# Optimization experiments

Measured on AMD Instinct MI355X. Metric: run time of the kernel, lower is better.

The kernel has to match this reference:

```python
import jax, jax.numpy as jnp
import numpy as np

B, N, M = 16, 4096, 1024
C2, C1 = 256, 128          # points2 channels (in_channel), points1 channels
MLP = [256, 256]
IN0 = C2 + C1              # use_points1=True concat


def setup_inputs() -> dict:
    key = jax.random.key(0)
    ks = jax.random.split(key, 8)
    inp = {
        "xyz1": jax.random.normal(ks[0], (B, 3, N), jnp.float32),
        "xyz2": jax.random.normal(ks[1], (B, 3, M), jnp.float32),
        "points1": jax.random.normal(ks[2], (B, C1, N), jnp.float32),
        "points2": jax.random.normal(ks[3], (B, C2, M), jnp.float32),
        # 1x1 Conv1d weights == dense matrices (out, in)
        "W1": jax.random.normal(ks[4], (MLP[0], IN0), jnp.float32) / np.sqrt(IN0),
        "b1": jnp.zeros((MLP[0],), jnp.float32),
        "W2": jax.random.normal(ks[5], (MLP[1], MLP[0]), jnp.float32) / np.sqrt(MLP[0]),
        "b2": jnp.zeros((MLP[1],), jnp.float32),
    }
    return inp


def _fp(xyz1, xyz2, points1, points2, W1, b1, W2, b2):
    # three_nn: squared pairwise distances via ||a||^2 + ||b||^2 - 2 a.b
    # xyz*: (B, 3, N/M)
    sq1 = jnp.sum(xyz1 * xyz1, axis=1)                 # (B, N)
    sq2 = jnp.sum(xyz2 * xyz2, axis=1)                 # (B, M)
    inner = jnp.einsum("bcn,bcm->bnm", xyz1, xyz2)     # (B, N, M)
    d2 = sq1[:, :, None] + sq2[:, None, :] - 2.0 * inner
    neg_d2, idx = jax.lax.top_k(-d2, 3)                # 3 smallest -> (B, N, 3)
    dist = jnp.sqrt(jnp.maximum(-neg_d2, 1e-20))       # Euclidean, like three_nn wrapper
    dist = jnp.maximum(dist, 1e-10)                    # torch.clamp_min
    recip = 1.0 / dist
    weight = recip / jnp.sum(recip, axis=2, keepdims=True)  # (B, N, 3)
    # three_interpolate: gather points2 at idx and weighted-sum
    gathered = jax.vmap(lambda p, i: p[:, i])(points2, idx)  # (B, C2, N, 3)
    interp = jnp.einsum("bcnk,bnk->bcn", gathered, weight)   # (B, C2, N)
    x = jnp.concatenate([interp, points1], axis=1)           # (B, C2+C1, N)
    # mlp_conv: 1x1 conv + relu (if_bn=False)
    x = jax.nn.relu(jnp.einsum("oc,bcn->bon", W1, x) + b1[None, :, None])
    x = jax.nn.relu(jnp.einsum("oc,bcn->bon", W2, x) + b2[None, :, None])
    return x


def reference(xyz1, xyz2, points1, points2, W1, b1, W2, b2):
    return _fp(xyz1, xyz2, points1, points2, W1, b1, W2, b2)
```

## Files before the change

kernel.cpp:

```cpp
#include <hip/hip_runtime.h>

#define B_  16
#define N_  4096
#define M_  1024
#define C1_ 128
#define C2_ 256
#define K0_ 384
#define O1_ 256
#define O2_ 256

typedef _Float16 half4  __attribute__((ext_vector_type(4)));
typedef _Float16 half8  __attribute__((ext_vector_type(8)));
typedef float    f32x4  __attribute__((ext_vector_type(4)));

__global__ __launch_bounds__(256)
void three_nn_kernel(const float* __restrict__ xyz1, const float* __restrict__ xyz2,
                     int* __restrict__ idxb, float* __restrict__ wb) {
    __shared__ float pts[8 * 516];
    int b = blockIdx.y;
    int t = threadIdx.x;
    {
        const float* src = xyz2 + (size_t)b * 3 * M_;
        int m0 = t * 4;
        f32x4 xv = *(const f32x4*)(src + m0);
        f32x4 yv = *(const f32x4*)(src + M_ + m0);
        f32x4 zv = *(const f32x4*)(src + 2 * M_ + m0);
        float* dst = pts + (m0 >> 7) * 516 + (m0 & 127) * 4;
#pragma unroll
        for (int jj = 0; jj < 4; ++jj) {
            f32x4 o = {xv[jj], yv[jj], zv[jj],
                       fmaf(xv[jj], xv[jj], fmaf(yv[jj], yv[jj], zv[jj] * zv[jj]))};
            *(f32x4*)(dst + jj * 4) = o;
        }
    }
    __syncthreads();
    int lane = t & 63;
    int c = lane & 7;
    int q = ((t >> 6) << 3) + (lane >> 3);
    int n = blockIdx.x * 32 + q;
    const float* qp = xyz1 + (size_t)b * 3 * N_;
    float px = qp[n], py = qp[N_ + n], pz = qp[2 * N_ + n];
    float px2 = -2.f * px, py2 = -2.f * py, pz2 = -2.f * pz;
    const float* base = pts + c * 516;
    float b0 = 1e30f, b1v = 1e30f, b2v = 1e30f;
    int i0 = 0, i1 = 0, i2 = 0;
    int mb = c * 128;
#pragma unroll 4
    for (int i = 0; i < 128; ++i) {
        f32x4 pv = *(const f32x4*)(base + i * 4);
        float d = fmaf(pv[0], px2, fmaf(pv[1], py2, fmaf(pv[2], pz2, pv[3])));
        int m = mb + i;
        bool c0 = d < b0, c1 = d < b1v, c2 = d < b2v;
        float nb1 = __builtin_amdgcn_fmed3f(d, b0, b1v);
        float nb2 = __builtin_amdgcn_fmed3f(d, b1v, b2v);
        i2 = c1 ? i1 : (c2 ? m : i2);
        i1 = c0 ? i0 : (c1 ? m : i1);
        i0 = c0 ? m : i0;
        b0 = fminf(b0, d);
        b1v = nb1; b2v = nb2;
    }
#pragma unroll
    for (int st = 1; st <= 4; st <<= 1) {
        float d0 = __shfl_xor(b0, st, 64);  int j0 = __shfl_xor(i0, st, 64);
        float d1 = __shfl_xor(b1v, st, 64); int j1 = __shfl_xor(i1, st, 64);
        float d2 = __shfl_xor(b2v, st, 64); int j2 = __shfl_xor(i2, st, 64);
#pragma unroll
        for (int e = 0; e < 3; ++e) {
            float d = (e == 0) ? d0 : (e == 1) ? d1 : d2;
            int   m = (e == 0) ? j0 : (e == 1) ? j1 : j2;
            bool c0 = d < b0, c1 = d < b1v, c2 = d < b2v;
            float nb1 = __builtin_amdgcn_fmed3f(d, b0, b1v);
            float nb2 = __builtin_amdgcn_fmed3f(d, b1v, b2v);
            i2 = c1 ? i1 : (c2 ? m : i2);
            i1 = c0 ? i0 : (c1 ? m : i1);
            i0 = c0 ? m : i0;
            b0 = fminf(b0, d);
            b1v = nb1; b2v = nb2;
        }
    }
    if ((lane & 7) == 0) {
        float sq1 = fmaf(px, px, fmaf(py, py, pz * pz));
        float e0 = fmaxf(sqrtf(fmaxf(b0 + sq1, 1e-20f)), 1e-10f);
        float e1 = fmaxf(sqrtf(fmaxf(b1v + sq1, 1e-20f)), 1e-10f);
        float e2 = fmaxf(sqrtf(fmaxf(b2v + sq1, 1e-20f)), 1e-10f);
        float r0 = 1.f / e0, r1 = 1.f / e1, r2 = 1.f / e2;
        float s = r0 + r1 + r2;
        size_t j = ((size_t)b * N_ + n) * 3;
        idxb[j] = i0; idxb[j + 1] = i1; idxb[j + 2] = i2;
        wb[j] = r0 / s; wb[j + 1] = r1 / s; wb[j + 2] = r2 / s;
    }
}

__global__ __launch_bounds__(256)
void convert_w_kernel(const float* __restrict__ W1, const float* __restrict__ W2,
                      _Float16* __restrict__ W1h, _Float16* __restrict__ W2h) {
    int t = blockIdx.x * 256 + threadIdx.x;
    if (t < O1_ * K0_) W1h[t] = (_Float16)W1[t];
    if (t < O2_ * O1_) W2h[t] = (_Float16)W2[t];
}

__global__ __launch_bounds__(256)
void transpose_f16_kernel(const float* __restrict__ in, _Float16* __restrict__ out,
                          int NP, size_t in_bstride, size_t out_bstride,
                          int out_rstride) {
    __shared__ float tile[64][65];
    int t = threadIdx.x;
    int nb = blockIdx.x * 64, cb = blockIdx.y * 64;
    const float* ib = in + blockIdx.z * in_bstride;
#pragma unroll
    for (int r = 0; r < 16; ++r) {
        int cc = r * 4 + (t >> 6);
        tile[cc][t & 63] = ib[(size_t)(cb + cc) * NP + nb + (t & 63)];
    }
    __syncthreads();
    _Float16* ob = out + blockIdx.z * out_bstride;
#pragma unroll
    for (int pass = 0; pass < 2; ++pass) {
        int id = pass * 256 + t;
        int nl = id >> 3;
        int c8 = (id & 7) * 8;
        half8 v;
#pragma unroll
        for (int jj = 0; jj < 8; ++jj) v[jj] = (_Float16)tile[c8 + jj][nl];
        *(half8*)(ob + (size_t)(nb + nl) * out_rstride + cb + c8) = v;
    }
}

__global__ __launch_bounds__(256, 2)
void gemm1_fused_kernel(const _Float16* __restrict__ p2T, const int* __restrict__ idxb,
                        const float* __restrict__ wb, const float* __restrict__ points1,
                        const _Float16* __restrict__ p1T,
                        const _Float16* __restrict__ W1h, const float* __restrict__ b1,
                        _Float16* __restrict__ Y1, int b0) {
    __shared__ char Xs[64 * 768];
    int b = b0 + blockIdx.y;
    int n0b = blockIdx.x * 64;
    int t = threadIdx.x;

    {
        int row = t >> 2, sub = t & 3;
        size_t j = ((size_t)b * N_ + n0b + row) * 3;
        int i0 = idxb[j], i1 = idxb[j + 1], i2 = idxb[j + 2];
        float w0 = wb[j], w1 = wb[j + 1], w2 = wb[j + 2];
        const _Float16* pb = p2T + (size_t)b * M_ * C2_;
        const half8* q0 = (const half8*)(pb + (size_t)i0 * C2_ + sub * 64);
        const half8* q1 = (const half8*)(pb + (size_t)i1 * C2_ + sub * 64);
        const half8* q2 = (const half8*)(pb + (size_t)i2 * C2_ + sub * 64);
        int rswz = (row & 7) << 4;
        char* xrow = Xs + row * 768;
#pragma unroll
        for (int x = 0; x < 8; ++x) {
            half8 a0 = q0[x], a1 = q1[x], a2 = q2[x];
            half8 v;
#pragma unroll
            for (int jj = 0; jj < 8; ++jj)
                v[jj] = (_Float16)(w0 * (float)a0[jj] + w1 * (float)a1[jj]
                                 + w2 * (float)a2[jj]);
            *(half8*)(xrow + ((sub * 128 + x * 16) ^ rswz)) = v;
        }
        if (p1T) {
            const half8* q3 = (const half8*)(p1T + ((size_t)b * N_ + n0b + row) * C1_ + sub * 32);
#pragma unroll
            for (int x = 0; x < 4; ++x) {
                half8 v = q3[x];
                *(half8*)(xrow + ((512 + sub * 64 + x * 16) ^ rswz)) = v;
            }
        } else {
            const float* pp = points1 + ((size_t)b * C1_ + sub * 32) * N_ + n0b + row;
#pragma unroll
            for (int x = 0; x < 4; ++x) {
                half8 v;
#pragma unroll
                for (int jj = 0; jj < 8; ++jj)
                    v[jj] = (_Float16)pp[(size_t)(x * 8 + jj) * N_];
                *(half8*)(xrow + ((512 + sub * 64 + x * 16) ^ rswz)) = v;
            }
        }
    }
    __syncthreads();

    int lane = t & 63, wv = t >> 6;
    int lr = lane & 15, lh = lane >> 4;
    int swz = (lr & 7) << 4;

    f32x4 acc[4][4];
#pragma unroll
    for (int of = 0; of < 4; ++of) {
        int o = wv * 64 + of * 16 + lh * 4;
        f32x4 bv = {b1[o], b1[o + 1], b1[o + 2], b1[o + 3]};
#pragma unroll
        for (int nf = 0; nf < 4; ++nf) acc[of][nf] = bv;
    }
    const _Float16* w1p = W1h + (size_t)(wv * 64 + lr) * K0_ + lh * 8;
#pragma unroll
    for (int k0 = 0; k0 < K0_; k0 += 32) {
        half8 bf[4];
#pragma unroll
        for (int nf = 0; nf < 4; ++nf)
            bf[nf] = *(const half8*)(Xs + (nf * 16 + lr) * 768 + ((k0 * 2 + lh * 16) ^ swz));
#pragma unroll
        for (int of = 0; of < 4; ++of) {
            half8 af = *(const half8*)(w1p + (size_t)of * 16 * K0_ + k0);
#pragma unroll
            for (int nf = 0; nf < 4; ++nf)
                acc[of][nf] = __builtin_amdgcn_mfma_f32_16x16x32_f16(af, bf[nf], acc[of][nf], 0, 0, 0);
        }
    }
    _Float16* yb = Y1 + ((size_t)b * N_ + n0b) * O1_;
#pragma unroll
    for (int of = 0; of < 4; ++of) {
#pragma unroll
        for (int nf = 0; nf < 4; ++nf) {
            int n = nf * 16 + lr;
            int o = wv * 64 + of * 16 + lh * 4;
            half4 h;
#pragma unroll
            for (int r = 0; r < 4; ++r) h[r] = (_Float16)fmaxf(acc[of][nf][r], 0.f);
            *(half4*)(yb + (size_t)n * O1_ + o) = h;
        }
    }
}

__global__ __launch_bounds__(256, 2)
void gemm2_kernel(const _Float16* __restrict__ Y1, const _Float16* __restrict__ W2h,
                  const float* __restrict__ b2, float* __restrict__ out, int b0) {
    int b = b0 + blockIdx.y;
    int n0b = blockIdx.x * 64;
    int t = threadIdx.x, lane = t & 63, wv = t >> 6;
    int lr = lane & 15, lh = lane >> 4;

    f32x4 acc[4][4];
#pragma unroll
    for (int of = 0; of < 4; ++of) {
        int o = wv * 64 + of * 16 + lh * 4;
        f32x4 bv = {b2[o], b2[o + 1], b2[o + 2], b2[o + 3]};
#pragma unroll
        for (int nf = 0; nf < 4; ++nf) acc[of][nf] = bv;
    }
    const _Float16* ap = W2h + (size_t)(wv * 64 + lr) * O1_ + lh * 8;
    const _Float16* bp = Y1 + ((size_t)b * N_ + n0b + lr) * O1_ + lh * 8;
#pragma unroll
    for (int k0 = 0; k0 < O1_; k0 += 32) {
        half8 af[4], bf[4];
#pragma unroll
        for (int of = 0; of < 4; ++of) af[of] = *(const half8*)(ap + (size_t)of * 16 * O1_ + k0);
#pragma unroll
        for (int nf = 0; nf < 4; ++nf) bf[nf] = *(const half8*)(bp + (size_t)nf * 16 * O1_ + k0);
#pragma unroll
        for (int of = 0; of < 4; ++of)
#pragma unroll
            for (int nf = 0; nf < 4; ++nf)
                acc[of][nf] = __builtin_amdgcn_mfma_f32_16x16x32_f16(af[of], bf[nf], acc[of][nf], 0, 0, 0);
    }
    float* ob = out + (size_t)b * O2_ * N_;
#pragma unroll
    for (int of = 0; of < 4; ++of) {
#pragma unroll
        for (int r = 0; r < 4; ++r) {
            int o2 = wv * 64 + of * 16 + lh * 4 + r;
#pragma unroll
            for (int nf = 0; nf < 4; ++nf)
                ob[(size_t)o2 * N_ + n0b + nf * 16 + lr] = fmaxf(acc[of][nf][r], 0.f);
        }
    }
}

extern "C" void kernel_launch(void* const* d_in, const int* in_sizes, int n_in,
                              void* d_out, int out_size, void* d_ws, size_t ws_size,
                              hipStream_t stream) {
    const float* xyz1    = (const float*)d_in[0];
    const float* xyz2    = (const float*)d_in[1];
    const float* points1 = (const float*)d_in[2];
    const float* points2 = (const float*)d_in[3];
    const float* W1      = (const float*)d_in[4];
    const float* b1      = (const float*)d_in[5];
    const float* W2      = (const float*)d_in[6];
    const float* b2      = (const float*)d_in[7];
    float* out = (float*)d_out;
    (void)in_sizes; (void)n_in; (void)out_size;

    char* p = (char*)d_ws;
    auto alloc = [&](size_t bytes) -> char* {
        char* r = p;
        p += (bytes + 255) & ~(size_t)255;
        return r;
    };
    _Float16* W1h  = (_Float16*)alloc((size_t)O1_ * K0_ * 2);
    _Float16* W2h  = (_Float16*)alloc((size_t)O2_ * O1_ * 2);
    int*      idxb = (int*)alloc((size_t)B_ * N_ * 3 * 4);
    float*    wbuf = (float*)alloc((size_t)B_ * N_ * 3 * 4);
    _Float16* p2T  = (_Float16*)alloc((size_t)B_ * M_ * C2_ * 2);
    size_t fixed = (size_t)(p - (char*)d_ws);

    size_t p1T_bytes = (size_t)B_ * N_ * C1_ * 2;
    size_t y1_full   = (size_t)B_ * N_ * O1_ * 2;
    size_t y1_per_b  = (size_t)N_ * O1_ * 2;

    _Float16* p1T = nullptr;
    _Float16* Y1  = nullptr;
    int G = B_;
    if (ws_size >= fixed + p1T_bytes + y1_full) {
        p1T = (_Float16*)alloc(p1T_bytes);
        Y1  = (_Float16*)alloc(y1_full);
    } else if (ws_size >= fixed + y1_full) {
        Y1 = (_Float16*)alloc(y1_full);
    } else {
        size_t avail = (ws_size > fixed) ? ws_size - fixed : y1_per_b;
        G = (int)(avail / y1_per_b);
        if (G < 1) G = 1;
        if (G > B_) G = B_;
        Y1 = (_Float16*)alloc((size_t)G * y1_per_b);
    }

    convert_w_kernel<<<dim3((O1_ * K0_ + 255) / 256), 256, 0, stream>>>(W1, W2, W1h, W2h);
    three_nn_kernel<<<dim3(N_ / 32, B_), 256, 0, stream>>>(xyz1, xyz2, idxb, wbuf);
    transpose_f16_kernel<<<dim3(M_ / 64, C2_ / 64, B_), 256, 0, stream>>>(
        points2, p2T, M_, (size_t)C2_ * M_, (size_t)M_ * C2_, C2_);
    if (p1T)
        transpose_f16_kernel<<<dim3(N_ / 64, C1_ / 64, B_), 256, 0, stream>>>(
            points1, p1T, N_, (size_t)C1_ * N_, (size_t)N_ * C1_, C1_);

    if (G >= B_) {
        gemm1_fused_kernel<<<dim3(N_ / 64, B_), 256, 0, stream>>>(
            p2T, idxb, wbuf, points1, p1T, W1h, b1, Y1, 0);
        gemm2_kernel<<<dim3(N_ / 64, B_), 256, 0, stream>>>(Y1, W2h, b2, out, 0);
    } else {
        for (int b0 = 0; b0 < B_; b0 += G) {
            int gc = (B_ - b0 < G) ? (B_ - b0) : G;
            gemm1_fused_kernel<<<dim3(N_ / 64, gc), 256, 0, stream>>>(
                p2T, idxb, wbuf, points1, p1T, W1h, b1, Y1, b0);
            gemm2_kernel<<<dim3(N_ / 64, gc), 256, 0, stream>>>(Y1, W2h, b2, out, b0);
        }
    }
}
```

Measured before the change: 234.7 us.

## Fuse both MLP GEMMs via LDS and merge prep kernels into one launch

Merges the three_nn, points2 transpose and weight conversion kernels into one prep kernel that dispatches on blockIdx.z. Fuses gemm1 and gemm2 so the ReLU'd first-layer activations stay in shared memory instead of a global Y1 buffer. Drops the points1 transpose path in favour of strided direct reads, adds software prefetch of the MFMA operands and an extra XOR term in the LDS swizzle, and raises launch bounds to 3 blocks per CU. The aim is to cut launch count and the global round trip of Y1. The cost is higher register pressure, and the strided points1 loads may be less coalesced.

```diff
diff --git a/kernel.cpp b/kernel.cpp
--- a/kernel.cpp
+++ b/kernel.cpp
@@ -13,61 +13,57 @@
 typedef _Float16 half8  __attribute__((ext_vector_type(8)));
 typedef float    f32x4  __attribute__((ext_vector_type(4)));
 
+__device__ __forceinline__ int swzX(int row, int kb) {
+    return row * 768 + (kb ^ ((row & 7) << 4) ^ (((kb >> 7) & 3) << 5));
+}
+__device__ __forceinline__ int swzY(int row, int kb) {
+    return row * 512 + (kb ^ ((row & 7) << 4));
+}
+
 __global__ __launch_bounds__(256)
-void three_nn_kernel(const float* __restrict__ xyz1, const float* __restrict__ xyz2,
-                     int* __restrict__ idxb, float* __restrict__ wb) {
-    __shared__ float pts[8 * 516];
-    int b = blockIdx.y;
+void prep_kernel(const float* __restrict__ xyz1, const float* __restrict__ xyz2,
+                 const float* __restrict__ points2,
+                 const float* __restrict__ W1, const float* __restrict__ W2,
+                 int* __restrict__ idxb, float* __restrict__ wb,
+                 _Float16* __restrict__ p2T,
+                 _Float16* __restrict__ W1h, _Float16* __restrict__ W2h) {
+    __shared__ __align__(16) char smem[16640];
     int t = threadIdx.x;
-    {
-        const float* src = xyz2 + (size_t)b * 3 * M_;
-        int m0 = t * 4;
-        f32x4 xv = *(const f32x4*)(src + m0);
-        f32x4 yv = *(const f32x4*)(src + M_ + m0);
-        f32x4 zv = *(const f32x4*)(src + 2 * M_ + m0);
-        float* dst = pts + (m0 >> 7) * 516 + (m0 & 127) * 4;
-#pragma unroll
-        for (int jj = 0; jj < 4; ++jj) {
-            f32x4 o = {xv[jj], yv[jj], zv[jj],
-                       fmaf(xv[jj], xv[jj], fmaf(yv[jj], yv[jj], zv[jj] * zv[jj]))};
-            *(f32x4*)(dst + jj * 4) = o;
-        }
-    }
-    __syncthreads();
-    int lane = t & 63;
-    int c = lane & 7;
-    int q = ((t >> 6) << 3) + (lane >> 3);
-    int n = blockIdx.x * 32 + q;
-    const float* qp = xyz1 + (size_t)b * 3 * N_;
-    float px = qp[n], py = qp[N_ + n], pz = qp[2 * N_ + n];
-    float px2 = -2.f * px, py2 = -2.f * py, pz2 = -2.f * pz;
-    const float* base = pts + c * 516;
-    float b0 = 1e30f, b1v = 1e30f, b2v = 1e30f;
-    int i0 = 0, i1 = 0, i2 = 0;
-    int mb = c * 128;
+
+    if (blockIdx.z == 0) {
+        float* pts = (float*)smem;
+        int b = blockIdx.y;
+        {
+            const float* src = xyz2 + (size_t)b * 3 * M_;
+            int m0 = t * 4;
+            f32x4 xv = *(const f32x4*)(src + m0);
+            f32x4 yv = *(const f32x4*)(src + M_ + m0);
+            f32x4 zv = *(const f32x4*)(src + 2 * M_ + m0);
+            float* dst = pts + (m0 >> 7) * 516 + (m0 & 127) * 4;
+#pragma unroll
+            for (int jj = 0; jj < 4; ++jj) {
+                f32x4 o = {xv[jj], yv[jj], zv[jj],
+                           fmaf(xv[jj], xv[jj], fmaf(yv[jj], yv[jj], zv[jj] * zv[jj]))};
+                *(f32x4*)(dst + jj * 4) = o;
+            }
+        }
+        __syncthreads();
+        int lane = t & 63;
+        int c = lane & 7;
+        int q = ((t >> 6) << 3) + (lane >> 3);
+        int n = blockIdx.x * 32 + q;
+        const float* qp = xyz1 + (size_t)b * 3 * N_;
+        float px = qp[n], py = qp[N_ + n], pz = qp[2 * N_ + n];
+        float px2 = -2.f * px, py2 = -2.f * py, pz2 = -2.f * pz;
+        const float* base = pts + c * 516;
+        float b0 = 1e30f, b1v = 1e30f, b2v = 1e30f;
+        int i0 = 0, i1 = 0, i2 = 0;
+        int mb = c * 128;
 #pragma unroll 4
-    for (int i = 0; i < 128; ++i) {
-        f32x4 pv = *(const f32x4*)(base + i * 4);
-        float d = fmaf(pv[0], px2, fmaf(pv[1], py2, fmaf(pv[2], pz2, pv[3])));
-        int m = mb + i;
-        bool c0 = d < b0, c1 = d < b1v, c2 = d < b2v;
-        float nb1 = __builtin_amdgcn_fmed3f(d, b0, b1v);
-        float nb2 = __builtin_amdgcn_fmed3f(d, b1v, b2v);
-        i2 = c1 ? i1 : (c2 ? m : i2);
-        i1 = c0 ? i0 : (c1 ? m : i1);
-        i0 = c0 ? m : i0;
-        b0 = fminf(b0, d);
-        b1v = nb1; b2v = nb2;
-    }
-#pragma unroll
-    for (int st = 1; st <= 4; st <<= 1) {
-        float d0 = __shfl_xor(b0, st, 64);  int j0 = __shfl_xor(i0, st, 64);
-        float d1 = __shfl_xor(b1v, st, 64); int j1 = __shfl_xor(i1, st, 64);
-        float d2 = __shfl_xor(b2v, st, 64); int j2 = __shfl_xor(i2, st, 64);
-#pragma unroll
-        for (int e = 0; e < 3; ++e) {
-            float d = (e == 0) ? d0 : (e == 1) ? d1 : d2;
-            int   m = (e == 0) ? j0 : (e == 1) ? j1 : j2;
+        for (int i = 0; i < 128; ++i) {
+            f32x4 pv = *(const f32x4*)(base + i * 4);
+            float d = fmaf(pv[0], px2, fmaf(pv[1], py2, fmaf(pv[2], pz2, pv[3])));
+            int m = mb + i;
             bool c0 = d < b0, c1 = d < b1v, c2 = d < b2v;
             float nb1 = __builtin_amdgcn_fmed3f(d, b0, b1v);
             float nb2 = __builtin_amdgcn_fmed3f(d, b1v, b2v);
@@ -77,63 +73,75 @@
             b0 = fminf(b0, d);
             b1v = nb1; b2v = nb2;
         }
-    }
-    if ((lane & 7) == 0) {
-        float sq1 = fmaf(px, px, fmaf(py, py, pz * pz));
-        float e0 = fmaxf(sqrtf(fmaxf(b0 + sq1, 1e-20f)), 1e-10f);
-        float e1 = fmaxf(sqrtf(fmaxf(b1v + sq1, 1e-20f)), 1e-10f);
-        float e2 = fmaxf(sqrtf(fmaxf(b2v + sq1, 1e-20f)), 1e-10f);
-        float r0 = 1.f / e0, r1 = 1.f / e1, r2 = 1.f / e2;
-        float s = r0 + r1 + r2;
-        size_t j = ((size_t)b * N_ + n) * 3;
-        idxb[j] = i0; idxb[j + 1] = i1; idxb[j + 2] = i2;
-        wb[j] = r0 / s; wb[j + 1] = r1 / s; wb[j + 2] = r2 / s;
-    }
-}
-
-__global__ __launch_bounds__(256)
-void convert_w_kernel(const float* __restrict__ W1, const float* __restrict__ W2,
-                      _Float16* __restrict__ W1h, _Float16* __restrict__ W2h) {
-    int t = blockIdx.x * 256 + threadIdx.x;
-    if (t < O1_ * K0_) W1h[t] = (_Float16)W1[t];
-    if (t < O2_ * O1_) W2h[t] = (_Float16)W2[t];
-}
-
-__global__ __launch_bounds__(256)
-void transpose_f16_kernel(const float* __restrict__ in, _Float16* __restrict__ out,
-                          int NP, size_t in_bstride, size_t out_bstride,
-                          int out_rstride) {
-    __shared__ float tile[64][65];
-    int t = threadIdx.x;
-    int nb = blockIdx.x * 64, cb = blockIdx.y * 64;
-    const float* ib = in + blockIdx.z * in_bstride;
-#pragma unroll
-    for (int r = 0; r < 16; ++r) {
-        int cc = r * 4 + (t >> 6);
-        tile[cc][t & 63] = ib[(size_t)(cb + cc) * NP + nb + (t & 63)];
-    }
-    __syncthreads();
-    _Float16* ob = out + blockIdx.z * out_bstride;
-#pragma unroll
-    for (int pass = 0; pass < 2; ++pass) {
-        int id = pass * 256 + t;
-        int nl = id >> 3;
-        int c8 = (id & 7) * 8;
-        half8 v;
-#pragma unroll
-        for (int jj = 0; jj < 8; ++jj) v[jj] = (_Float16)tile[c8 + jj][nl];
-        *(half8*)(ob + (size_t)(nb + nl) * out_rstride + cb + c8) = v;
-    }
-}
-
-__global__ __launch_bounds__(256, 2)
-void gemm1_fused_kernel(const _Float16* __restrict__ p2T, const int* __restrict__ idxb,
-                        const float* __restrict__ wb, const float* __restrict__ points1,
-                        const _Float16* __restrict__ p1T,
-                        const _Float16* __restrict__ W1h, const float* __restrict__ b1,
-                        _Float16* __restrict__ Y1, int b0) {
-    __shared__ char Xs[64 * 768];
-    int b = b0 + blockIdx.y;
+#pragma unroll
+        for (int st = 1; st <= 4; st <<= 1) {
+            float d0 = __shfl_xor(b0, st, 64);  int j0 = __shfl_xor(i0, st, 64);
+            float d1 = __shfl_xor(b1v, st, 64); int j1 = __shfl_xor(i1, st, 64);
+            float d2 = __shfl_xor(b2v, st, 64); int j2 = __shfl_xor(i2, st, 64);
+#pragma unroll
+            for (int e = 0; e < 3; ++e) {
+                float d = (e == 0) ? d0 : (e == 1) ? d1 : d2;
+                int   m = (e == 0) ? j0 : (e == 1) ? j1 : j2;
+                bool c0 = d < b0, c1 = d < b1v, c2 = d < b2v;
+                float nb1 = __builtin_amdgcn_fmed3f(d, b0, b1v);
+                float nb2 = __builtin_amdgcn_fmed3f(d, b1v, b2v);
+                i2 = c1 ? i1 : (c2 ? m : i2);
+                i1 = c0 ? i0 : (c1 ? m : i1);
+                i0 = c0 ? m : i0;
+                b0 = fminf(b0, d);
+                b1v = nb1; b2v = nb2;
+            }
+        }
+        if ((lane & 7) == 0) {
+            float sq1 = fmaf(px, px, fmaf(py, py, pz * pz));
+            float e0 = fmaxf(sqrtf(fmaxf(b0 + sq1, 1e-20f)), 1e-10f);
+            float e1 = fmaxf(sqrtf(fmaxf(b1v + sq1, 1e-20f)), 1e-10f);
+            float e2 = fmaxf(sqrtf(fmaxf(b2v + sq1, 1e-20f)), 1e-10f);
+            float r0 = 1.f / e0, r1 = 1.f / e1, r2 = 1.f / e2;
+            float s = r0 + r1 + r2;
+            size_t j = ((size_t)b * N_ + n) * 3;
+            idxb[j] = i0; idxb[j + 1] = i1; idxb[j + 2] = i2;
+            wb[j] = r0 / s; wb[j + 1] = r1 / s; wb[j + 2] = r2 / s;
+        }
+    } else if (blockIdx.z == 1) {
+        if (blockIdx.x >= 64) return;
+        float (*tile)[65] = (float(*)[65])smem;
+        int nb = (blockIdx.x & 15) * 64, cb = (blockIdx.x >> 4) * 64;
+        const float* ib = points2 + (size_t)blockIdx.y * C2_ * M_;
+#pragma unroll
+        for (int r = 0; r < 16; ++r) {
+            int cc = r * 4 + (t >> 6);
+            tile[cc][t & 63] = ib[(size_t)(cb + cc) * M_ + nb + (t & 63)];
+        }
+        __syncthreads();
+        _Float16* ob = p2T + (size_t)blockIdx.y * M_ * C2_;
+#pragma unroll
+        for (int pass = 0; pass < 2; ++pass) {
+            int id = pass * 256 + t;
+            int nl = id >> 3;
+            int c8 = (id & 7) * 8;
+            half8 v;
+#pragma unroll
+            for (int jj = 0; jj < 8; ++jj) v[jj] = (_Float16)tile[c8 + jj][nl];
+            *(half8*)(ob + (size_t)(nb + nl) * C2_ + cb + c8) = v;
+        }
+    } else {
+        int id = blockIdx.y * 128 + blockIdx.x;
+        if (id >= 384) return;
+        int g = id * 256 + t;
+        if (g < O1_ * K0_) W1h[g] = (_Float16)W1[g];
+        if (g < O2_ * O1_) W2h[g] = (_Float16)W2[g];
+    }
+}
+
+__global__ __launch_bounds__(256, 3)
+void fused_mlp_kernel(const _Float16* __restrict__ p2T, const int* __restrict__ idxb,
+                      const float* __restrict__ wb, const float* __restrict__ points1,
+                      const _Float16* __restrict__ W1h, const float* __restrict__ b1,
+                      const _Float16* __restrict__ W2h, const float* __restrict__ b2,
+                      float* __restrict__ out) {
+    __shared__ __align__(16) char Xs[64 * 768];
+    int b = blockIdx.y;
     int n0b = blockIdx.x * 64;
     int t = threadIdx.x;
 
@@ -146,8 +154,6 @@
         const half8* q0 = (const half8*)(pb + (size_t)i0 * C2_ + sub * 64);
         const half8* q1 = (const half8*)(pb + (size_t)i1 * C2_ + sub * 64);
         const half8* q2 = (const half8*)(pb + (size_t)i2 * C2_ + sub * 64);
-        int rswz = (row & 7) << 4;
-        char* xrow = Xs + row * 768;
 #pragma unroll
         for (int x = 0; x < 8; ++x) {
             half8 a0 = q0[x], a1 = q1[x], a2 = q2[x];
@@ -156,32 +162,22 @@
             for (int jj = 0; jj < 8; ++jj)
                 v[jj] = (_Float16)(w0 * (float)a0[jj] + w1 * (float)a1[jj]
                                  + w2 * (float)a2[jj]);
-            *(half8*)(xrow + ((sub * 128 + x * 16) ^ rswz)) = v;
-        }
-        if (p1T) {
-            const half8* q3 = (const half8*)(p1T + ((size_t)b * N_ + n0b + row) * C1_ + sub * 32);
-#pragma unroll
-            for (int x = 0; x < 4; ++x) {
-                half8 v = q3[x];
-                *(half8*)(xrow + ((512 + sub * 64 + x * 16) ^ rswz)) = v;
-            }
-        } else {
-            const float* pp = points1 + ((size_t)b * C1_ + sub * 32) * N_ + n0b + row;
-#pragma unroll
-            for (int x = 0; x < 4; ++x) {
-                half8 v;
-#pragma unroll
-                for (int jj = 0; jj < 8; ++jj)
-                    v[jj] = (_Float16)pp[(size_t)(x * 8 + jj) * N_];
-                *(half8*)(xrow + ((512 + sub * 64 + x * 16) ^ rswz)) = v;
-            }
+            *(half8*)(Xs + swzX(row, sub * 128 + x * 16)) = v;
+        }
+        const float* pp = points1 + ((size_t)b * C1_ + sub * 32) * N_ + n0b + row;
+#pragma unroll
+        for (int x = 0; x < 4; ++x) {
+            half8 v;
+#pragma unroll
+            for (int jj = 0; jj < 8; ++jj)
+                v[jj] = (_Float16)pp[(size_t)(x * 8 + jj) * N_];
+            *(half8*)(Xs + swzX(row, 512 + sub * 64 + x * 16)) = v;
         }
     }
     __syncthreads();
 
     int lane = t & 63, wv = t >> 6;
     int lr = lane & 15, lh = lane >> 4;
-    int swz = (lr & 7) << 4;
 
     f32x4 acc[4][4];
 #pragma unroll
@@ -192,65 +188,89 @@
         for (int nf = 0; nf < 4; ++nf) acc[of][nf] = bv;
     }
     const _Float16* w1p = W1h + (size_t)(wv * 64 + lr) * K0_ + lh * 8;
-#pragma unroll
-    for (int k0 = 0; k0 < K0_; k0 += 32) {
-        half8 bf[4];
-#pragma unroll
-        for (int nf = 0; nf < 4; ++nf)
-            bf[nf] = *(const half8*)(Xs + (nf * 16 + lr) * 768 + ((k0 * 2 + lh * 16) ^ swz));
-#pragma unroll
-        for (int of = 0; of < 4; ++of) {
-            half8 af = *(const half8*)(w1p + (size_t)of * 16 * K0_ + k0);
-#pragma unroll
-            for (int nf = 0; nf < 4; ++nf)
-                acc[of][nf] = __builtin_amdgcn_mfma_f32_16x16x32_f16(af, bf[nf], acc[of][nf], 0, 0, 0);
-        }
-    }
-    _Float16* yb = Y1 + ((size_t)b * N_ + n0b) * O1_;
+    half8 af[4], bf[4];
+#pragma unroll
+    for (int of = 0; of < 4; ++of) af[of] = *(const half8*)(w1p + (size_t)of * 16 * K0_);
+#pragma unroll
+    for (int nf = 0; nf < 4; ++nf) bf[nf] = *(const half8*)(Xs + swzX(nf * 16 + lr, lh * 16));
+#pragma unroll
+    for (int ks = 0; ks < 12; ++ks) {
+        half8 naf[4], nbf[4];
+        if (ks < 11) {
+            int kk = (ks + 1) * 32;
+#pragma unroll
+            for (int of = 0; of < 4; ++of)
+                naf[of] = *(const half8*)(w1p + (size_t)of * 16 * K0_ + kk);
+#pragma unroll
+            for (int nf = 0; nf < 4; ++nf)
+                nbf[nf] = *(const half8*)(Xs + swzX(nf * 16 + lr, kk * 2 + lh * 16));
+        }
+#pragma unroll
+        for (int of = 0; of < 4; ++of)
+#pragma unroll
+            for (int nf = 0; nf < 4; ++nf)
+                acc[of][nf] = __builtin_amdgcn_mfma_f32_16x16x32_f16(af[of], bf[nf], acc[of][nf], 0, 0, 0);
+        if (ks < 11) {
+#pragma unroll
+            for (int of = 0; of < 4; ++of) af[of] = naf[of];
+#pragma unroll
+            for (int nf = 0; nf < 4; ++nf) bf[nf] = nbf[nf];
+        }
+    }
+    __syncthreads();
+
+    char* Ys = Xs;
 #pragma unroll
     for (int of = 0; of < 4; ++of) {
 #pragma unroll
         for (int nf = 0; nf < 4; ++nf) {
-            int n = nf * 16 + lr;
-            int o = wv * 64 + of * 16 + lh * 4;
+            int rn = nf * 16 + lr;
+            int obyte = (wv * 64 + of * 16 + lh * 4) * 2;
             half4 h;
 #pragma unroll
             for (int r = 0; r < 4; ++r) h[r] = (_Float16)fmaxf(acc[of][nf][r], 0.f);
-            *(half4*)(yb + (size_t)n * O1_ + o) = h;
-        }
-    }
-}
-
-__global__ __launch_bounds__(256, 2)
-void gemm2_kernel(const _Float16* __restrict__ Y1, const _Float16* __restrict__ W2h,
-                  const float* __restrict__ b2, float* __restrict__ out, int b0) {
-    int b = b0 + blockIdx.y;
-    int n0b = blockIdx.x * 64;
-    int t = threadIdx.x, lane = t & 63, wv = t >> 6;
-    int lr = lane & 15, lh = lane >> 4;
-
-    f32x4 acc[4][4];
+            *(half4*)(Ys + swzY(rn, obyte)) = h;
+        }
+    }
+    __syncthreads();
+
+    f32x4 acc2[4][4];
 #pragma unroll
     for (int of = 0; of < 4; ++of) {
         int o = wv * 64 + of * 16 + lh * 4;
         f32x4 bv = {b2[o], b2[o + 1], b2[o + 2], b2[o + 3]};
 #pragma unroll
-        for (int nf = 0; nf < 4; ++nf) acc[of][nf] = bv;
-    }
-    const _Float16* ap = W2h + (size_t)(wv * 64 + lr) * O1_ + lh * 8;
-    const _Float16* bp = Y1 + ((size_t)b * N_ + n0b + lr) * O1_ + lh * 8;
-#pragma unroll
-    for (int k0 = 0; k0 < O1_; k0 += 32) {
-        half8 af[4], bf[4];
-#pragma unroll
-        for (int of = 0; of < 4; ++of) af[of] = *(const half8*)(ap + (size_t)of * 16 * O1_ + k0);
-#pragma unroll
-        for (int nf = 0; nf < 4; ++nf) bf[nf] = *(const half8*)(bp + (size_t)nf * 16 * O1_ + k0);
+        for (int nf = 0; nf < 4; ++nf) acc2[of][nf] = bv;
+    }
+    const _Float16* w2p = W2h + (size_t)(wv * 64 + lr) * O1_ + lh * 8;
+    half8 af2[4], bf2[4];
+#pragma unroll
+    for (int of = 0; of < 4; ++of) af2[of] = *(const half8*)(w2p + (size_t)of * 16 * O1_);
+#pragma unroll
+    for (int nf = 0; nf < 4; ++nf) bf2[nf] = *(const half8*)(Ys + swzY(nf * 16 + lr, lh * 16));
+#pragma unroll
+    for (int ks = 0; ks < 8; ++ks) {
+        half8 naf[4], nbf[4];
+        if (ks < 7) {
+            int kk = (ks + 1) * 32;
+#pragma unroll
+            for (int of = 0; of < 4; ++of)
+                naf[of] = *(const half8*)(w2p + (size_t)of * 16 * O1_ + kk);
+#pragma unroll
+            for (int nf = 0; nf < 4; ++nf)
+                nbf[nf] = *(const half8*)(Ys + swzY(nf * 16 + lr, kk * 2 + lh * 16));
+        }
 #pragma unroll
         for (int of = 0; of < 4; ++of)
 #pragma unroll
             for (int nf = 0; nf < 4; ++nf)
-                acc[of][nf] = __builtin_amdgcn_mfma_f32_16x16x32_f16(af[of], bf[nf], acc[of][nf], 0, 0, 0);
+                acc2[of][nf] = __builtin_amdgcn_mfma_f32_16x16x32_f16(af2[of], bf2[nf], acc2[of][nf], 0, 0, 0);
+        if (ks < 7) {
+#pragma unroll
+            for (int of = 0; of < 4; ++of) af2[of] = naf[of];
+#pragma unroll
+            for (int nf = 0; nf < 4; ++nf) bf2[nf] = nbf[nf];
+        }
     }
     float* ob = out + (size_t)b * O2_ * N_;
 #pragma unroll
@@ -260,7 +280,7 @@
             int o2 = wv * 64 + of * 16 + lh * 4 + r;
 #pragma unroll
             for (int nf = 0; nf < 4; ++nf)
-                ob[(size_t)o2 * N_ + n0b + nf * 16 + lr] = fmaxf(acc[of][nf][r], 0.f);
+                ob[(size_t)o2 * N_ + n0b + nf * 16 + lr] = fmaxf(acc2[of][nf][r], 0.f);
         }
     }
 }
@@ -277,7 +297,7 @@
     const float* W2      = (const float*)d_in[6];
     const float* b2      = (const float*)d_in[7];
     float* out = (float*)d_out;
-    (void)in_sizes; (void)n_in; (void)out_size;
+    (void)in_sizes; (void)n_in; (void)out_size; (void)ws_size;
 
     char* p = (char*)d_ws;
     auto alloc = [&](size_t bytes) -> char* {
@@ -290,46 +310,9 @@
     int*      idxb = (int*)alloc((size_t)B_ * N_ * 3 * 4);
     float*    wbuf = (float*)alloc((size_t)B_ * N_ * 3 * 4);
     _Float16* p2T  = (_Float16*)alloc((size_t)B_ * M_ * C2_ * 2);
-    size_t fixed = (size_t)(p - (char*)d_ws);
-
-    size_t p1T_bytes = (size_t)B_ * N_ * C1_ * 2;
-    size_t y1_full   = (size_t)B_ * N_ * O1_ * 2;
-    size_t y1_per_b  = (size_t)N_ * O1_ * 2;
-
-    _Float16* p1T = nullptr;
-    _Float16* Y1  = nullptr;
-    int G = B_;
-    if (ws_size >= fixed + p1T_bytes + y1_full) {
-        p1T = (_Float16*)alloc(p1T_bytes);
-        Y1  = (_Float16*)alloc(y1_full);
-    } else if (ws_size >= fixed + y1_full) {
-        Y1 = (_Float16*)alloc(y1_full);
-    } else {
-        size_t avail = (ws_size > fixed) ? ws_size - fixed : y1_per_b;
-        G = (int)(avail / y1_per_b);
-        if (G < 1) G = 1;
-        if (G > B_) G = B_;
-        Y1 = (_Float16*)alloc((size_t)G * y1_per_b);
-    }
-
-    convert_w_kernel<<<dim3((O1_ * K0_ + 255) / 256), 256, 0, stream>>>(W1, W2, W1h, W2h);
-    three_nn_kernel<<<dim3(N_ / 32, B_), 256, 0, stream>>>(xyz1, xyz2, idxb, wbuf);
-    transpose_f16_kernel<<<dim3(M_ / 64, C2_ / 64, B_), 256, 0, stream>>>(
-        points2, p2T, M_, (size_t)C2_ * M_, (size_t)M_ * C2_, C2_);
-    if (p1T)
-        transpose_f16_kernel<<<dim3(N_ / 64, C1_ / 64, B_), 256, 0, stream>>>(
-            points1, p1T, N_, (size_t)C1_ * N_, (size_t)N_ * C1_, C1_);
-
-    if (G >= B_) {
-        gemm1_fused_kernel<<<dim3(N_ / 64, B_), 256, 0, stream>>>(
-            p2T, idxb, wbuf, points1, p1T, W1h, b1, Y1, 0);
-        gemm2_kernel<<<dim3(N_ / 64, B_), 256, 0, stream>>>(Y1, W2h, b2, out, 0);
-    } else {
-        for (int b0 = 0; b0 < B_; b0 += G) {
-            int gc = (B_ - b0 < G) ? (B_ - b0) : G;
-            gemm1_fused_kernel<<<dim3(N_ / 64, gc), 256, 0, stream>>>(
-                p2T, idxb, wbuf, points1, p1T, W1h, b1, Y1, b0);
-            gemm2_kernel<<<dim3(N_ / 64, gc), 256, 0, stream>>>(Y1, W2h, b2, out, b0);
-        }
-    }
-}
+
+    prep_kernel<<<dim3(128, 16, 3), 256, 0, stream>>>(
+        xyz1, xyz2, points2, W1, W2, idxb, wbuf, p2T, W1h, W2h);
+    fused_mlp_kernel<<<dim3(N_ / 64, B_), 256, 0, stream>>>(
+        p2T, idxb, wbuf, points1, W1h, b1, W2h, b2, out);
+}
```

New measurement: 198.5 us. 1.18x faster.
